# Optimization experiments

Hardware: AMD Instinct MI355X
Metric: run time of the kernel (lower is better)

Reference implementation:

```python
import jax, jax.numpy as jnp
import numpy as np

H = 8       # hidden size (nn.GRU(1, 8, 2))
T = 131072  # sequence length
B = 1       # batch (fixed by hidden_state buffer shape (2,1,8))


def setup_inputs() -> dict:
    key = jax.random.key(0)
    ks = jax.random.split(key, 12)
    s = 1.0 / np.sqrt(H)  # torch default init scale ~ U(-1/sqrt(H), 1/sqrt(H))
    def w(k, shape):
        return jax.random.uniform(k, shape, dtype=jnp.float32, minval=-s, maxval=s)
    return {
        "x": jax.random.normal(ks[0], (T, B, 1), dtype=jnp.float32),
        "h0": jax.random.normal(ks[1], (2, B, H), dtype=jnp.float32),
        "w_ih_l0": w(ks[2], (3 * H, 1)),
        "w_hh_l0": w(ks[3], (3 * H, H)),
        "b_ih_l0": w(ks[4], (3 * H,)),
        "b_hh_l0": w(ks[5], (3 * H,)),
        "w_ih_l1": w(ks[6], (3 * H, H)),
        "w_hh_l1": w(ks[7], (3 * H, H)),
        "b_ih_l1": w(ks[8], (3 * H,)),
        "b_hh_l1": w(ks[9], (3 * H,)),
        "w_lin": w(ks[10], (1, H)),
        "b_lin": w(ks[11], (1,)),
    }


def _gru_layer(x_seq, h0, w_ih, w_hh, b_ih, b_hh):
    """PyTorch GRU layer: x_seq (T,B,I), h0 (B,H) -> outputs (T,B,H)."""
    # Precompute input-side gate projections for all timesteps (hoisted GEMM).
    gx = jnp.einsum('tbi,gi->tbg', x_seq, w_ih) + b_ih  # (T,B,3H)

    def step(h, gxt):
        gh = h @ w_hh.T + b_hh                                  # (B,3H)
        r = jax.nn.sigmoid(gxt[..., :H] + gh[..., :H])
        z = jax.nn.sigmoid(gxt[..., H:2 * H] + gh[..., H:2 * H])
        n = jnp.tanh(gxt[..., 2 * H:] + r * gh[..., 2 * H:])
        h_new = (1.0 - z) * n + z * h
        return h_new, h_new

    h_last, ys = jax.lax.scan(step, h0, gx)
    return ys, h_last


def reference(x, h0, w_ih_l0, w_hh_l0, b_ih_l0, b_hh_l0,
              w_ih_l1, w_hh_l1, b_ih_l1, b_hh_l1, w_lin, b_lin):
    y0, _ = _gru_layer(x, h0[0], w_ih_l0, w_hh_l0, b_ih_l0, b_hh_l0)
    y1, _ = _gru_layer(y0, h0[1], w_ih_l1, w_hh_l1, b_ih_l1, b_hh_l1)
    # Original: x.view(-1) then Linear(8,1) (valid only when T*B==1).
    # Generalized per-timestep readout; identical math for T*B==1.
    out = y1.reshape(-1, H) @ w_lin.T + b_lin  # (T*B, 1)
    return out
```

## Files before the change

kernel.cpp:

```cpp
#include <hip/hip_runtime.h>

#define H 8
#define T_LEN 131072
#define CHUNK_L 32
#define WARM 32
#define NCHUNK (T_LEN / CHUNK_L)
#define CPW 4
#define CPB 4
#define NBLK (NCHUNK / CPB)
#define SX_LEN 80
#define SX_OFF 3
#define HSTRIDE 264

__device__ __forceinline__ float fast_rcp(float x) { return __builtin_amdgcn_rcpf(x); }
__device__ __forceinline__ float exp2_f(float x) {
#if __has_builtin(__builtin_amdgcn_exp2f)
    return __builtin_amdgcn_exp2f(x);
#else
    return exp2f(x);
#endif
}
template<int N>
__device__ __forceinline__ float row_ror(float v) {
    return __int_as_float(__builtin_amdgcn_update_dpp(
        0, __float_as_int(v), 0x120 + N, 0xF, 0xF, true));
}

__global__ __launch_bounds__(64, 1) void gru_chunk_kernel(
    const float* __restrict__ x, const float* __restrict__ hinit,
    const float* __restrict__ wih0, const float* __restrict__ whh0,
    const float* __restrict__ bih0, const float* __restrict__ bhh0,
    const float* __restrict__ wih1, const float* __restrict__ whh1,
    const float* __restrict__ bih1, const float* __restrict__ bhh1,
    const float* __restrict__ wlin, const float* __restrict__ blin,
    float* __restrict__ out)
{
    const int tid = threadIdx.x;
    const int p = tid & 15;
    const int rrow = tid >> 4;
    const int c = blockIdx.x * CPB + rrow;
    const int C = c * CHUNK_L;
    const int tf = C - WARM;
    const int s_reset = (tf <= 0) ? -tf : -1;
    const bool has_reset = (blockIdx.x == 0);

    alignas(16) __shared__ float sx[CPB][SX_LEN];
    alignas(16) __shared__ float Wbuf[16][4][16];
    __shared__ float bbuf[16][4];
    __shared__ float wxbuf[16][3];
    alignas(16) __shared__ float histS[CPB * HSTRIDE];

    {
        const int ci = tid >> 4, j0 = tid & 15;
        const int tfc = (blockIdx.x * CPB + ci) * CHUNK_L - WARM;
#pragma unroll
        for (int i = 0; i < 5; i++) {
            const int idx = j0 + 16 * i;
            const int xi = tfc + idx - SX_OFF;
            sx[ci][idx] = (xi >= 0 && xi < T_LEN) ? x[xi] : 0.0f;
        }
    }

    {
        const int u = tid & 15, g = tid >> 4;
        const int ukk = u & 7, uL = u >> 3;
        const int rowi = (g == 0) ? ukk : (g == 1) ? (H + ukk) : (2 * H + ukk);
        float Ws[16];
#pragma unroll
        for (int j = 0; j < 16; j++) Ws[j] = 0.0f;
        float b = 0.0f, wxv = 0.0f;
        if (g <= 1) {
            if (uL == 0) {
#pragma unroll
                for (int j = 0; j < 8; j++) Ws[j] = whh0[rowi * H + j];
                b = bih0[rowi] + bhh0[rowi];
                wxv = wih0[rowi];
            } else {
#pragma unroll
                for (int j = 0; j < 8; j++) {
                    Ws[j]     = wih1[rowi * H + j];
                    Ws[8 + j] = whh1[rowi * H + j];
                }
                b = bih1[rowi] + bhh1[rowi];
            }
        } else if (g == 2) {
            if (uL == 0) { b = bih0[rowi]; wxv = wih0[rowi]; }
            else {
#pragma unroll
                for (int j = 0; j < 8; j++) Ws[j] = wih1[rowi * H + j];
                b = bih1[rowi];
            }
        } else {
            if (uL == 0) {
#pragma unroll
                for (int j = 0; j < 8; j++) Ws[j] = whh0[rowi * H + j];
                b = bhh0[rowi];
            } else {
#pragma unroll
                for (int j = 0; j < 8; j++) Ws[8 + j] = whh1[rowi * H + j];
                b = bhh1[rowi];
            }
        }
        const float scale = (g < 2) ? -1.442695040888963f : 2.885390081777927f;
#pragma unroll
        for (int N = 0; N < 16; N++) Wbuf[u][g][N] = Ws[(u - N) & 15] * scale;
        bbuf[u][g] = b * scale;
        if (g < 3) wxbuf[u][g] = wxv * scale;
    }
    __syncthreads();

    float Wg[4][16];
#pragma unroll
    for (int g = 0; g < 4; g++) {
        const float4* wp = (const float4*)&Wbuf[p][g][0];
        float4 q0 = wp[0], q1 = wp[1], q2 = wp[2], q3 = wp[3];
        Wg[g][0]=q0.x;  Wg[g][1]=q0.y;  Wg[g][2]=q0.z;  Wg[g][3]=q0.w;
        Wg[g][4]=q1.x;  Wg[g][5]=q1.y;  Wg[g][6]=q1.z;  Wg[g][7]=q1.w;
        Wg[g][8]=q2.x;  Wg[g][9]=q2.y;  Wg[g][10]=q2.z; Wg[g][11]=q2.w;
        Wg[g][12]=q3.x; Wg[g][13]=q3.y; Wg[g][14]=q3.z; Wg[g][15]=q3.w;
    }
    const float br = bbuf[p][0], bz = bbuf[p][1], bni = bbuf[p][2], bnh = bbuf[p][3];
    const float wxr = wxbuf[p][0], wxz = wxbuf[p][1], wxn = wxbuf[p][2];
    const float hval_init = hinit[p];

    const bool hlane = (p >= 8);
    float* histc = &histS[rrow * HSTRIDE];
    const float* sxc = &sx[rrow][0];

    float hv = 0.0f;

#define STEP(XV, SCUR, STORE)                                            \
    do {                                                                 \
        if (has_reset) hv = ((SCUR) == s_reset) ? hval_init : hv;        \
        float S[16];                                                     \
        S[0] = hv;                                                       \
        S[1]  = row_ror<1>(hv);   S[2]  = row_ror<2>(hv);                \
        S[3]  = row_ror<3>(hv);   S[4]  = row_ror<4>(hv);                \
        S[5]  = row_ror<5>(hv);   S[6]  = row_ror<6>(hv);                \
        S[7]  = row_ror<7>(hv);   S[8]  = row_ror<8>(hv);                \
        S[9]  = row_ror<9>(hv);   S[10] = row_ror<10>(hv);               \
        S[11] = row_ror<11>(hv);  S[12] = row_ror<12>(hv);               \
        S[13] = row_ror<13>(hv);  S[14] = row_ror<14>(hv);               \
        S[15] = row_ror<15>(hv);                                         \
        float ar0 = fmaf(wxr, (XV), br), ar1 = 0.0f;                     \
        float az0 = fmaf(wxz, (XV), bz), az1 = 0.0f;                     \
        float ai0 = fmaf(wxn, (XV), bni), ai1 = 0.0f;                    \
        float ah0 = bnh, ah1 = 0.0f;                                     \
        _Pragma("unroll")                                                \
        for (int N = 0; N < 8; N++) {                                    \
            ar0 = fmaf(Wg[0][N], S[N], ar0);                             \
            az0 = fmaf(Wg[1][N], S[N], az0);                             \
            ai0 = fmaf(Wg[2][N], S[N], ai0);                             \
            ah0 = fmaf(Wg[3][N], S[N], ah0);                             \
            ar1 = fmaf(Wg[0][8 + N], S[8 + N], ar1);                     \
            az1 = fmaf(Wg[1][8 + N], S[8 + N], az1);                     \
            ai1 = fmaf(Wg[2][8 + N], S[8 + N], ai1);                     \
            ah1 = fmaf(Wg[3][8 + N], S[8 + N], ah1);                     \
        }                                                                \
        float ar = ar0 + ar1, az = az0 + az1;                            \
        float ai = ai0 + ai1, ah = ah0 + ah1;                            \
        float r_ = fast_rcp(1.0f + exp2_f(ar));                         \
        float z_ = fast_rcp(1.0f + exp2_f(az));                         \
        float tn = fmaf(r_, ah, ai);                                     \
        float nn = fmaf(-2.0f, fast_rcp(1.0f + exp2_f(tn)), 1.0f);       \
        float hnew = fmaf(z_, hv - nn, nn);                              \
        if (has_reset) {                                                 \
            hv = (((SCUR) == s_reset) && hlane) ? hv : hnew;             \
        } else {                                                         \
            hv = hnew;                                                   \
        }                                                                \
        if (STORE && hlane) histc[((SCUR) - (WARM + 1)) * 8 + (p - 8)] = hv; \
    } while (0)

    float xv0 = sxc[SX_OFF];
    float4 xg = *(const float4*)&sxc[4];
    float xq0 = xg.x, xq1 = xg.y, xq2 = xg.z, xq3 = xg.w;

    STEP(xv0, 0, false);
    int s = 1;
    for (; s <= WARM - 3; s += 4) {
        float4 xn = *(const float4*)&sxc[s + 7];
        STEP(xq0, s + 0, false);
        STEP(xq1, s + 1, false);
        STEP(xq2, s + 2, false);
        STEP(xq3, s + 3, false);
        xq0 = xn.x; xq1 = xn.y; xq2 = xn.z; xq3 = xn.w;
    }
    for (; s <= WARM + CHUNK_L - 3; s += 4) {
        float4 xn = *(const float4*)&sxc[s + 7];
        STEP(xq0, s + 0, true);
        STEP(xq1, s + 1, true);
        STEP(xq2, s + 2, true);
        STEP(xq3, s + 3, true);
        xq0 = xn.x; xq1 = xn.y; xq2 = xn.z; xq3 = xn.w;
    }
#undef STEP

    __syncthreads();
    {
        float wl[8];
#pragma unroll
        for (int e = 0; e < 8; e++) wl[e] = wlin[e];
        const float bl = blin[0];
#pragma unroll
        for (int h = 0; h < 2; h++) {
            const int t2 = tid + 64 * h;
            const int q = t2 >> 5, row = t2 & 31;
            const float4* hp = (const float4*)&histS[q * HSTRIDE + row * 8];
            float4 hA = hp[0], hB = hp[1];
            float ov = bl;
            ov = fmaf(wl[0], hA.x, ov); ov = fmaf(wl[1], hA.y, ov);
            ov = fmaf(wl[2], hA.z, ov); ov = fmaf(wl[3], hA.w, ov);
            ov = fmaf(wl[4], hB.x, ov); ov = fmaf(wl[5], hB.y, ov);
            ov = fmaf(wl[6], hB.z, ov); ov = fmaf(wl[7], hB.w, ov);
            out[blockIdx.x * (CPB * CHUNK_L) + t2] = ov;
        }
    }
}

extern "C" void kernel_launch(void* const* d_in, const int* in_sizes, int n_in,
                              void* d_out, int out_size, void* d_ws, size_t ws_size,
                              hipStream_t stream) {
    (void)in_sizes; (void)n_in; (void)d_ws; (void)ws_size; (void)out_size;
    const float* x    = (const float*)d_in[0];
    const float* h0   = (const float*)d_in[1];
    const float* wih0 = (const float*)d_in[2];
    const float* whh0 = (const float*)d_in[3];
    const float* bih0 = (const float*)d_in[4];
    const float* bhh0 = (const float*)d_in[5];
    const float* wih1 = (const float*)d_in[6];
    const float* whh1 = (const float*)d_in[7];
    const float* bih1 = (const float*)d_in[8];
    const float* bhh1 = (const float*)d_in[9];
    const float* wlin = (const float*)d_in[10];
    const float* blin = (const float*)d_in[11];
    float* out = (float*)d_out;

    gru_chunk_kernel<<<NBLK, 64, 0, stream>>>(
        x, h0, wih0, whh0, bih0, bhh0, wih1, whh1, bih1, bhh1, wlin, blin, out);
}
```

Before: 23.57 us.

## Pack GRU gate FMAs into v_pk_fma_f32 pairs and shorten warmup

Pairs the r/z and n-input/n-hidden gate accumulators into two-wide float vectors so the recurrent matvec can be emitted as packed FMAs, roughly halving the FMA instruction count on the serial critical path. It also shortens the per-chunk warmup from 32 to 24 steps, which cuts redundant recurrence work. The shorter warmup relies on the hidden state converging within fewer steps and may reduce accuracy. Packed FMA also needs the broadcast operand, which may cost extra moves.

```diff
diff --git a/kernel.cpp b/kernel.cpp
--- a/kernel.cpp
+++ b/kernel.cpp
@@ -3,14 +3,15 @@
 #define H 8
 #define T_LEN 131072
 #define CHUNK_L 32
-#define WARM 32
+#define WARM 24
 #define NCHUNK (T_LEN / CHUNK_L)
-#define CPW 4
 #define CPB 4
 #define NBLK (NCHUNK / CPB)
 #define SX_LEN 80
 #define SX_OFF 3
 #define HSTRIDE 264
+
+typedef float v2f __attribute__((ext_vector_type(2)));
 
 __device__ __forceinline__ float fast_rcp(float x) { return __builtin_amdgcn_rcpf(x); }
 __device__ __forceinline__ float exp2_f(float x) {
@@ -18,6 +19,13 @@
     return __builtin_amdgcn_exp2f(x);
 #else
     return exp2f(x);
+#endif
+}
+__device__ __forceinline__ v2f pk_fma(v2f a, v2f b, v2f c) {
+#if __has_builtin(__builtin_elementwise_fma)
+    return __builtin_elementwise_fma(a, b, c);
+#else
+    return a * b + c;
 #endif
 }
 template<int N>
@@ -109,18 +117,25 @@
     }
     __syncthreads();
 
-    float Wg[4][16];
-#pragma unroll
-    for (int g = 0; g < 4; g++) {
-        const float4* wp = (const float4*)&Wbuf[p][g][0];
-        float4 q0 = wp[0], q1 = wp[1], q2 = wp[2], q3 = wp[3];
-        Wg[g][0]=q0.x;  Wg[g][1]=q0.y;  Wg[g][2]=q0.z;  Wg[g][3]=q0.w;
-        Wg[g][4]=q1.x;  Wg[g][5]=q1.y;  Wg[g][6]=q1.z;  Wg[g][7]=q1.w;
-        Wg[g][8]=q2.x;  Wg[g][9]=q2.y;  Wg[g][10]=q2.z; Wg[g][11]=q2.w;
-        Wg[g][12]=q3.x; Wg[g][13]=q3.y; Wg[g][14]=q3.z; Wg[g][15]=q3.w;
-    }
-    const float br = bbuf[p][0], bz = bbuf[p][1], bni = bbuf[p][2], bnh = bbuf[p][3];
-    const float wxr = wxbuf[p][0], wxz = wxbuf[p][1], wxn = wxbuf[p][2];
+    v2f WRZ[16], WNX[16];
+    {
+        const float4* w0 = (const float4*)&Wbuf[p][0][0];
+        const float4* w1 = (const float4*)&Wbuf[p][1][0];
+        const float4* w2 = (const float4*)&Wbuf[p][2][0];
+        const float4* w3 = (const float4*)&Wbuf[p][3][0];
+#pragma unroll
+        for (int q4 = 0; q4 < 4; q4++) {
+            float4 a = w0[q4], b = w1[q4], cc = w2[q4], d = w3[q4];
+            WRZ[4*q4+0] = v2f{a.x, b.x};  WNX[4*q4+0] = v2f{cc.x, d.x};
+            WRZ[4*q4+1] = v2f{a.y, b.y};  WNX[4*q4+1] = v2f{cc.y, d.y};
+            WRZ[4*q4+2] = v2f{a.z, b.z};  WNX[4*q4+2] = v2f{cc.z, d.z};
+            WRZ[4*q4+3] = v2f{a.w, b.w};  WNX[4*q4+3] = v2f{cc.w, d.w};
+        }
+    }
+    const v2f bRZ  = v2f{bbuf[p][0], bbuf[p][1]};
+    const v2f bNX  = v2f{bbuf[p][2], bbuf[p][3]};
+    const v2f wxRZ = v2f{wxbuf[p][0], wxbuf[p][1]};
+    const v2f wxNX = v2f{wxbuf[p][2], 0.0f};
     const float hval_init = hinit[p];
 
     const bool hlane = (p >= 8);
@@ -141,27 +156,25 @@
         S[9]  = row_ror<9>(hv);   S[10] = row_ror<10>(hv);               \
         S[11] = row_ror<11>(hv);  S[12] = row_ror<12>(hv);               \
         S[13] = row_ror<13>(hv);  S[14] = row_ror<14>(hv);               \
+        const v2f xs = v2f{(XV), (XV)};                                  \
+        v2f aRZ0 = pk_fma(wxRZ, xs, bRZ);                                \
+        v2f aNX0 = pk_fma(wxNX, xs, bNX);                                \
+        v2f aRZ1 = v2f{0.0f, 0.0f}, aNX1 = v2f{0.0f, 0.0f};              \
         S[15] = row_ror<15>(hv);                                         \
-        float ar0 = fmaf(wxr, (XV), br), ar1 = 0.0f;                     \
-        float az0 = fmaf(wxz, (XV), bz), az1 = 0.0f;                     \
-        float ai0 = fmaf(wxn, (XV), bni), ai1 = 0.0f;                    \
-        float ah0 = bnh, ah1 = 0.0f;                                     \
         _Pragma("unroll")                                                \
         for (int N = 0; N < 8; N++) {                                    \
-            ar0 = fmaf(Wg[0][N], S[N], ar0);                             \
-            az0 = fmaf(Wg[1][N], S[N], az0);                             \
-            ai0 = fmaf(Wg[2][N], S[N], ai0);                             \
-            ah0 = fmaf(Wg[3][N], S[N], ah0);                             \
-            ar1 = fmaf(Wg[0][8 + N], S[8 + N], ar1);                     \
-            az1 = fmaf(Wg[1][8 + N], S[8 + N], az1);                     \
-            ai1 = fmaf(Wg[2][8 + N], S[8 + N], ai1);                     \
-            ah1 = fmaf(Wg[3][8 + N], S[8 + N], ah1);                     \
+            const v2f sA = v2f{S[N], S[N]};                              \
+            const v2f sB = v2f{S[8 + N], S[8 + N]};                      \
+            aRZ0 = pk_fma(WRZ[N], sA, aRZ0);                             \
+            aNX0 = pk_fma(WNX[N], sA, aNX0);                             \
+            aRZ1 = pk_fma(WRZ[8 + N], sB, aRZ1);                         \
+            aNX1 = pk_fma(WNX[8 + N], sB, aNX1);                         \
         }                                                                \
-        float ar = ar0 + ar1, az = az0 + az1;                            \
-        float ai = ai0 + ai1, ah = ah0 + ah1;                            \
-        float r_ = fast_rcp(1.0f + exp2_f(ar));                         \
-        float z_ = fast_rcp(1.0f + exp2_f(az));                         \
-        float tn = fmaf(r_, ah, ai);                                     \
+        const v2f aRZ = aRZ0 + aRZ1;                                     \
+        const v2f aNX = aNX0 + aNX1;                                     \
+        float r_ = fast_rcp(1.0f + exp2_f(aRZ.x));                       \
+        float z_ = fast_rcp(1.0f + exp2_f(aRZ.y));                       \
+        float tn = fmaf(r_, aNX.y, aNX.x);                               \
         float nn = fmaf(-2.0f, fast_rcp(1.0f + exp2_f(tn)), 1.0f);       \
         float hnew = fmaf(z_, hv - nn, nn);                              \
         if (has_reset) {                                                 \
```

New measurement: 20.37 us. -13.6%, faster.
